# Performance work log

Measured on AMD Instinct MI355X. Metric: run time of the kernel, lower is better.

## Reference

```python
import jax, jax.numpy as jnp
import numpy as np


def _gcn_layer(ann, adj, Wa, ba, W2, b2):
    # ann: [B,N,F], adj: [B,E,N,N], Wa: [E,F,U], ba: [E,U], W2: [F,U], b2: [U]
    # per-edge-type linear, fused as one batched einsum -> [B,E,N,U]
    h = jnp.einsum('bnf,efu->benu', ann, Wa) + ba[None, :, None, :]
    # adjacency matmul per edge type: [B,E,N,N] @ [B,E,N,U]
    h = jnp.einsum('benm,bemu->benu', adj, h)
    # sum over edge types + residual linear + activation (tanh)
    out = h.sum(axis=1) + jnp.einsum('bnf,fu->bnu', ann, W2) + b2
    return jnp.tanh(out)


def setup_inputs() -> dict:
    key = jax.random.key(0)
    ks = jax.random.split(key, 10)
    B, N, F, E, U = 32, 1024, 32, 4, 32
    s = 1.0 / np.sqrt(F)
    s1 = 1.0 / np.sqrt(F + U)
    return {
        'n_tensor': jax.random.normal(ks[0], (B, N, F), dtype=jnp.float32),
        'adj_tensor': jax.random.uniform(ks[1], (B, E, N, N), dtype=jnp.float32),
        'W_adj0': jax.random.normal(ks[2], (E, F, U), dtype=jnp.float32) * s,
        'b_adj0': jax.random.normal(ks[3], (E, U), dtype=jnp.float32) * s,
        'W2_0': jax.random.normal(ks[4], (F, U), dtype=jnp.float32) * s,
        'b2_0': jax.random.normal(ks[5], (U,), dtype=jnp.float32) * s,
        'W_adj1': jax.random.normal(ks[6], (E, F + U, U), dtype=jnp.float32) * s1,
        'b_adj1': jax.random.normal(ks[7], (E, U), dtype=jnp.float32) * s1,
        'W2_1': jax.random.normal(ks[8], (F + U, U), dtype=jnp.float32) * s1,
        'b2_1': jax.random.normal(ks[9], (U,), dtype=jnp.float32) * s1,
    }


def reference(n_tensor, adj_tensor, W_adj0, b_adj0, W2_0, b2_0,
              W_adj1, b_adj1, W2_1, b2_1):
    # layer 0: h_tensor is None -> annotations = n_tensor
    h = _gcn_layer(n_tensor, adj_tensor, W_adj0, b_adj0, W2_0, b2_0)
    # layer 1: annotations = cat(n_tensor, hidden)
    ann1 = jnp.concatenate([n_tensor, h], axis=-1)
    h = _gcn_layer(ann1, adj_tensor, W_adj1, b_adj1, W2_1, b2_1)
    return h
```

## Files before the change

### kernel.cpp

```cpp
#include <hip/hip_runtime.h>
#include <math.h>

#define Nn 1024
#define Ee 4
#define Uu 32

template <int F, int FA>
__global__ __launch_bounds__(256) void pre_kernel(
    const float* __restrict__ annA, const float* __restrict__ annB,
    const float* __restrict__ Wa, const float* __restrict__ ba,
    const float* __restrict__ W2, const float* __restrict__ b2,
    float* __restrict__ hpre_t, float* __restrict__ res)
{
    const int e = blockIdx.y;
    __shared__ float wlds[F * Uu];
    __shared__ float blds[Uu];
    const int tid = threadIdx.x;
    const float* wsrc = (e < 4) ? (Wa + (size_t)e * F * Uu) : W2;
    const float* bsrc = (e < 4) ? (ba + (size_t)e * Uu) : b2;
    for (int i = tid; i < F * Uu; i += 256) wlds[i] = wsrc[i];
    if (tid < Uu) blds[tid] = bsrc[tid];
    __syncthreads();

    const int g = blockIdx.x * 256 + tid;
    const int b = g >> 10;
    const int n = g & 1023;

    float4 a4[F / 4];
    {
        const float4* rA = (const float4*)(annA + (size_t)g * FA);
#pragma unroll
        for (int i = 0; i < FA / 4; ++i) a4[i] = rA[i];
        if constexpr (F > FA) {
            const float4* rB = (const float4*)(annB + (size_t)g * (F - FA));
#pragma unroll
            for (int i = 0; i < (F - FA) / 4; ++i) a4[FA / 4 + i] = rB[i];
        }
    }

    float4 acc[8];
    const float4* bb = (const float4*)blds;
#pragma unroll
    for (int uq = 0; uq < 8; ++uq) acc[uq] = bb[uq];
    const float4* w4 = (const float4*)wlds;
#pragma unroll
    for (int f4 = 0; f4 < F / 4; ++f4) {
        const float4 av = a4[f4];
#pragma unroll
        for (int c = 0; c < 4; ++c) {
            const float s = (c == 0) ? av.x : (c == 1) ? av.y : (c == 2) ? av.z : av.w;
#pragma unroll
            for (int uq = 0; uq < 8; ++uq) {
                const float4 w = w4[(f4 * 4 + c) * 8 + uq];
                acc[uq].x = fmaf(s, w.x, acc[uq].x);
                acc[uq].y = fmaf(s, w.y, acc[uq].y);
                acc[uq].z = fmaf(s, w.z, acc[uq].z);
                acc[uq].w = fmaf(s, w.w, acc[uq].w);
            }
        }
    }
    if (e < 4) {
        float* dst = hpre_t + ((size_t)(b * 4 + e) * Uu) * Nn + n;
#pragma unroll
        for (int uq = 0; uq < 8; ++uq) {
            dst[(uq * 4 + 0) * Nn] = acc[uq].x;
            dst[(uq * 4 + 1) * Nn] = acc[uq].y;
            dst[(uq * 4 + 2) * Nn] = acc[uq].z;
            dst[(uq * 4 + 3) * Nn] = acc[uq].w;
        }
    } else {
        float4* dst = (float4*)(res + (size_t)g * Uu);
#pragma unroll
        for (int uq = 0; uq < 8; ++uq) dst[uq] = acc[uq];
    }
}

__global__ __launch_bounds__(256, 2) void gcn_main_kernel(
    const float* __restrict__ adj,
    const float* __restrict__ hpre_t,
    const float* __restrict__ res,
    float* __restrict__ out)
{
    __shared__ float part[4][8][Uu];

    const int bid = blockIdx.x;
    const int swz = (bid & 7) * 512 + (bid >> 3);
    const int b = swz >> 7;
    const int n0 = (swz & 127) * 8;
    const int tid = threadIdx.x;
    const int w = tid >> 6;
    const int lane = tid & 63;
    const int gu = lane >> 4;
    const int ms = lane & 15;

    const float* adjb = adj + (size_t)b * Ee * Nn * Nn;
    const float* hpb  = hpre_t + (size_t)b * Ee * Uu * Nn;
    const int mbase = w * 256 + ms * 4;

    float acc[8][8];
#pragma unroll
    for (int r = 0; r < 8; ++r)
#pragma unroll
        for (int j = 0; j < 8; ++j) acc[r][j] = 0.f;

#pragma unroll 2
    for (int it = 0; it < 16; ++it) {
        const int e = it >> 2, sub = it & 3;
        const float* ap = adjb + ((size_t)e * Nn + n0) * Nn + mbase + sub * 64;
        const float* hp = hpb + ((size_t)e * Uu + gu * 8) * Nn + mbase + sub * 64;
        float4 av[8], hv[8];
#pragma unroll
        for (int r = 0; r < 8; ++r) av[r] = *(const float4*)(ap + (size_t)r * Nn);
#pragma unroll
        for (int j = 0; j < 8; ++j) hv[j] = *(const float4*)(hp + (size_t)j * Nn);
#pragma unroll
        for (int j = 0; j < 8; ++j)
#pragma unroll
            for (int r = 0; r < 8; ++r) {
                float t0 = fmaf(av[r].x, hv[j].x, acc[r][j]);
                t0 = fmaf(av[r].y, hv[j].y, t0);
                t0 = fmaf(av[r].z, hv[j].z, t0);
                acc[r][j] = fmaf(av[r].w, hv[j].w, t0);
            }
    }

#pragma unroll
    for (int r = 0; r < 8; ++r)
#pragma unroll
        for (int j = 0; j < 8; ++j) {
            float v = acc[r][j];
            v += __shfl_xor(v, 1);
            v += __shfl_xor(v, 2);
            v += __shfl_xor(v, 4);
            v += __shfl_xor(v, 8);
            acc[r][j] = v;
        }

#pragma unroll
    for (int r = 0; r < 8; ++r) {
        if (ms == r) {
#pragma unroll
            for (int j = 0; j < 8; ++j) part[w][r][gu * 8 + j] = acc[r][j];
        }
    }
    __syncthreads();

    {
        const int r = tid >> 5, u = tid & 31;
        const float v = part[0][r][u] + part[1][r][u] + part[2][r][u] + part[3][r][u];
        const size_t oi = ((size_t)b * Nn + n0 + r) * Uu + u;
        out[oi] = tanhf(v + res[oi]);
    }
}

extern "C" void kernel_launch(void* const* d_in, const int* in_sizes, int n_in,
                              void* d_out, int out_size, void* d_ws, size_t ws_size,
                              hipStream_t stream)
{
    const float* n_tensor = (const float*)d_in[0];
    const float* adj      = (const float*)d_in[1];
    const float* W_adj0   = (const float*)d_in[2];
    const float* b_adj0   = (const float*)d_in[3];
    const float* W2_0     = (const float*)d_in[4];
    const float* b2_0     = (const float*)d_in[5];
    const float* W_adj1   = (const float*)d_in[6];
    const float* b_adj1   = (const float*)d_in[7];
    const float* W2_1     = (const float*)d_in[8];
    const float* b2_1     = (const float*)d_in[9];
    float* outp = (float*)d_out;

    float* ws   = (float*)d_ws;
    float* hpre = ws;
    float* resb = ws + (size_t)4 * 1024 * 1024;
    float* h0   = ws + (size_t)5 * 1024 * 1024;

    dim3 pre_grid(128, 5);

    pre_kernel<32, 32><<<pre_grid, 256, 0, stream>>>(n_tensor, nullptr, W_adj0, b_adj0,
                                                     W2_0, b2_0, hpre, resb);
    gcn_main_kernel<<<4096, 256, 0, stream>>>(adj, hpre, resb, h0);

    pre_kernel<64, 32><<<pre_grid, 256, 0, stream>>>(n_tensor, h0, W_adj1, b_adj1,
                                                     W2_1, b2_1, hpre, resb);
    gcn_main_kernel<<<4096, 256, 0, stream>>>(adj, hpre, resb, outp);
}
```

Baseline: 518.8 us.

## Stage hidden features in LDS and enlarge row tile per block

The adjacency-matmul kernel now processes 32 rows per 512-thread block. Each stage copies a 32x512 slice of the transformed hidden features into LDS with global_load_lds, and every wave reads it from there instead of re-fetching it from global memory. Each wave owns 4 full rows across all m, which removes the cross-wave LDS reduction and allows a vectorized tanh/residual epilogue. This cuts redundant h traffic but adds per-stage barriers and 64KB of LDS per block, which may limit occupancy. Adjacency streaming is unchanged.

```diff
diff --git a/kernel.cpp b/kernel.cpp
--- a/kernel.cpp
+++ b/kernel.cpp
@@ -4,6 +4,8 @@
 #define Nn 1024
 #define Ee 4
 #define Uu 32
+#define STAGE_M 512
+#define BLOCK_ROWS 32
 
 template <int F, int FA>
 __global__ __launch_bounds__(256) void pre_kernel(
@@ -75,57 +77,76 @@
     }
 }
 
-__global__ __launch_bounds__(256, 2) void gcn_main_kernel(
+__global__ __launch_bounds__(512, 4) void gcn_main_kernel(
     const float* __restrict__ adj,
     const float* __restrict__ hpre_t,
     const float* __restrict__ res,
     float* __restrict__ out)
 {
-    __shared__ float part[4][8][Uu];
+    __shared__ float hlds[Uu * STAGE_M];
 
     const int bid = blockIdx.x;
-    const int swz = (bid & 7) * 512 + (bid >> 3);
-    const int b = swz >> 7;
-    const int n0 = (swz & 127) * 8;
+    const int swz = (bid & 7) * 128 + (bid >> 3);
+    const int b = swz >> 5;
+    const int n0 = (swz & 31) * BLOCK_ROWS;
     const int tid = threadIdx.x;
     const int w = tid >> 6;
     const int lane = tid & 63;
     const int gu = lane >> 4;
     const int ms = lane & 15;
+    const int wrow = n0 + w * 4;
 
     const float* adjb = adj + (size_t)b * Ee * Nn * Nn;
     const float* hpb  = hpre_t + (size_t)b * Ee * Uu * Nn;
-    const int mbase = w * 256 + ms * 4;
-
-    float acc[8][8];
-#pragma unroll
-    for (int r = 0; r < 8; ++r)
+
+    float acc[4][8];
+#pragma unroll
+    for (int r = 0; r < 4; ++r)
 #pragma unroll
         for (int j = 0; j < 8; ++j) acc[r][j] = 0.f;
 
-#pragma unroll 2
-    for (int it = 0; it < 16; ++it) {
-        const int e = it >> 2, sub = it & 3;
-        const float* ap = adjb + ((size_t)e * Nn + n0) * Nn + mbase + sub * 64;
-        const float* hp = hpb + ((size_t)e * Uu + gu * 8) * Nn + mbase + sub * 64;
-        float4 av[8], hv[8];
-#pragma unroll
-        for (int r = 0; r < 8; ++r) av[r] = *(const float4*)(ap + (size_t)r * Nn);
-#pragma unroll
-        for (int j = 0; j < 8; ++j) hv[j] = *(const float4*)(hp + (size_t)j * Nn);
-#pragma unroll
-        for (int j = 0; j < 8; ++j)
-#pragma unroll
-            for (int r = 0; r < 8; ++r) {
-                float t0 = fmaf(av[r].x, hv[j].x, acc[r][j]);
-                t0 = fmaf(av[r].y, hv[j].y, t0);
-                t0 = fmaf(av[r].z, hv[j].z, t0);
-                acc[r][j] = fmaf(av[r].w, hv[j].w, t0);
+    for (int s = 0; s < 8; ++s) {
+        const int e = s >> 1;
+        const int m0 = (s & 1) * STAGE_M;
+
+        {
+            const float* hsrc = hpb + ((size_t)e * Uu + w * 4) * Nn + m0 + lane * 4;
+#pragma unroll
+            for (int uu = 0; uu < 4; ++uu) {
+#pragma unroll
+                for (int seg = 0; seg < 2; ++seg) {
+                    __builtin_amdgcn_global_load_lds(
+                        (const __attribute__((address_space(1))) void*)(hsrc + (size_t)uu * Nn + seg * 256),
+                        (__attribute__((address_space(3))) void*)(&hlds[(w * 4 + uu) * STAGE_M + seg * 256]),
+                        16, 0, 0);
+                }
             }
-    }
-
-#pragma unroll
-    for (int r = 0; r < 8; ++r)
+        }
+        __syncthreads();
+
+#pragma unroll
+        for (int c = 0; c < 8; ++c) {
+            const float* ap = adjb + ((size_t)e * Nn + wrow) * Nn + m0 + c * 64 + ms * 4;
+            float4 av[4];
+#pragma unroll
+            for (int r = 0; r < 4; ++r) av[r] = *(const float4*)(ap + (size_t)r * Nn);
+#pragma unroll
+            for (int j = 0; j < 8; ++j) {
+                const float4 hv = *(const float4*)(&hlds[(gu * 8 + j) * STAGE_M + c * 64 + ms * 4]);
+#pragma unroll
+                for (int r = 0; r < 4; ++r) {
+                    float t0 = fmaf(av[r].x, hv.x, acc[r][j]);
+                    t0 = fmaf(av[r].y, hv.y, t0);
+                    t0 = fmaf(av[r].z, hv.z, t0);
+                    acc[r][j] = fmaf(av[r].w, hv.w, t0);
+                }
+            }
+        }
+        __syncthreads();
+    }
+
+#pragma unroll
+    for (int r = 0; r < 4; ++r)
 #pragma unroll
         for (int j = 0; j < 8; ++j) {
             float v = acc[r][j];
@@ -137,19 +158,25 @@
         }
 
 #pragma unroll
-    for (int r = 0; r < 8; ++r) {
+    for (int r = 0; r < 4; ++r) {
         if (ms == r) {
-#pragma unroll
-            for (int j = 0; j < 8; ++j) part[w][r][gu * 8 + j] = acc[r][j];
-        }
-    }
-    __syncthreads();
-
-    {
-        const int r = tid >> 5, u = tid & 31;
-        const float v = part[0][r][u] + part[1][r][u] + part[2][r][u] + part[3][r][u];
-        const size_t oi = ((size_t)b * Nn + n0 + r) * Uu + u;
-        out[oi] = tanhf(v + res[oi]);
+            const int n = wrow + r;
+            const float* rp = res + ((size_t)b * Nn + n) * Uu + gu * 8;
+            float* op = out + ((size_t)b * Nn + n) * Uu + gu * 8;
+            const float4 r0 = *(const float4*)(rp);
+            const float4 r1 = *(const float4*)(rp + 4);
+            float4 o0, o1;
+            o0.x = tanhf(acc[r][0] + r0.x);
+            o0.y = tanhf(acc[r][1] + r0.y);
+            o0.z = tanhf(acc[r][2] + r0.z);
+            o0.w = tanhf(acc[r][3] + r0.w);
+            o1.x = tanhf(acc[r][4] + r1.x);
+            o1.y = tanhf(acc[r][5] + r1.y);
+            o1.z = tanhf(acc[r][6] + r1.z);
+            o1.w = tanhf(acc[r][7] + r1.w);
+            *(float4*)(op) = o0;
+            *(float4*)(op + 4) = o1;
+        }
     }
 }
 
@@ -178,9 +205,9 @@
 
     pre_kernel<32, 32><<<pre_grid, 256, 0, stream>>>(n_tensor, nullptr, W_adj0, b_adj0,
                                                      W2_0, b2_0, hpre, resb);
-    gcn_main_kernel<<<4096, 256, 0, stream>>>(adj, hpre, resb, h0);
+    gcn_main_kernel<<<1024, 512, 0, stream>>>(adj, hpre, resb, h0);
 
     pre_kernel<64, 32><<<pre_grid, 256, 0, stream>>>(n_tensor, h0, W_adj1, b_adj1,
                                                      W2_1, b2_1, hpre, resb);
-    gcn_main_kernel<<<4096, 256, 0, stream>>>(adj, hpre, resb, outp);
+    gcn_main_kernel<<<1024, 512, 0, stream>>>(adj, hpre, resb, outp);
 }
```

Result: faster. 445.2 us (-14.2%).

## Stage hidden features in LDS and widen GCN blocks to 32 adjacency rows

Applied to the files above, without the earlier changes.

The adjacency-matmul kernel now processes 32 output rows per block instead of 8, so it launches 1024 blocks instead of 4096. Each 256-column chunk of the transposed hidden features is staged in shared memory and shared by all four waves, with the next chunk prefetched into registers while the current one is consumed. This cuts the repeated L2/global reads of the hidden-feature matrix that every 8-row block used to make, leaving the kernel closer to being limited by streaming the adjacency tensor. In exchange each thread holds 64 accumulators, the kernel uses 32 KB of shared memory and two barriers per step, and the occupancy hint was dropped, which may lower occupancy and latency hiding.

```diff
diff --git a/kernel.cpp b/kernel.cpp
--- a/kernel.cpp
+++ b/kernel.cpp
@@ -4,6 +4,7 @@
 #define Nn 1024
 #define Ee 4
 #define Uu 32
+#define BLOCK_ROWS 32
 
 template <int F, int FA>
 __global__ __launch_bounds__(256) void pre_kernel(
@@ -75,81 +76,127 @@
     }
 }
 
-__global__ __launch_bounds__(256, 2) void gcn_main_kernel(
+__global__ __launch_bounds__(256) void gcn_main_kernel(
     const float* __restrict__ adj,
     const float* __restrict__ hpre_t,
     const float* __restrict__ res,
     float* __restrict__ out)
 {
-    __shared__ float part[4][8][Uu];
+    __shared__ float buf[Uu * 256];
 
     const int bid = blockIdx.x;
-    const int swz = (bid & 7) * 512 + (bid >> 3);
-    const int b = swz >> 7;
-    const int n0 = (swz & 127) * 8;
+    const int swz = (bid & 7) * 128 + (bid >> 3);
+    const int b = swz >> 5;
+    const int n0 = (swz & 31) * BLOCK_ROWS;
     const int tid = threadIdx.x;
     const int w = tid >> 6;
     const int lane = tid & 63;
-    const int gu = lane >> 4;
     const int ms = lane & 15;
+    const int rg = lane >> 4;
+    const int wrow = n0 + w * 8;
 
     const float* adjb = adj + (size_t)b * Ee * Nn * Nn;
     const float* hpb  = hpre_t + (size_t)b * Ee * Uu * Nn;
-    const int mbase = w * 256 + ms * 4;
-
-    float acc[8][8];
-#pragma unroll
-    for (int r = 0; r < 8; ++r)
-#pragma unroll
-        for (int j = 0; j < 8; ++j) acc[r][j] = 0.f;
-
-#pragma unroll 2
-    for (int it = 0; it < 16; ++it) {
-        const int e = it >> 2, sub = it & 3;
-        const float* ap = adjb + ((size_t)e * Nn + n0) * Nn + mbase + sub * 64;
-        const float* hp = hpb + ((size_t)e * Uu + gu * 8) * Nn + mbase + sub * 64;
-        float4 av[8], hv[8];
-#pragma unroll
-        for (int r = 0; r < 8; ++r) av[r] = *(const float4*)(ap + (size_t)r * Nn);
-#pragma unroll
-        for (int j = 0; j < 8; ++j) hv[j] = *(const float4*)(hp + (size_t)j * Nn);
-#pragma unroll
-        for (int j = 0; j < 8; ++j)
-#pragma unroll
-            for (int r = 0; r < 8; ++r) {
-                float t0 = fmaf(av[r].x, hv[j].x, acc[r][j]);
-                t0 = fmaf(av[r].y, hv[j].y, t0);
-                t0 = fmaf(av[r].z, hv[j].z, t0);
-                acc[r][j] = fmaf(av[r].w, hv[j].w, t0);
+
+    const int uh = tid >> 3, qb = tid & 7;
+    float4* buf4 = (float4*)buf;
+
+    float accA[32], accB[32];
+#pragma unroll
+    for (int u = 0; u < 32; ++u) { accA[u] = 0.f; accB[u] = 0.f; }
+
+    float4 hr[8];
+
+    {
+        const float* hs = hpb + (size_t)uh * Nn + qb * 4;
+#pragma unroll
+        for (int k = 0; k < 8; ++k) hr[k] = *(const float4*)(hs + k * 32);
+    }
+
+    for (int s = 0; s < 16; ++s) {
+        const int e = s >> 2, mq = s & 3;
+
+        asm volatile("s_waitcnt lgkmcnt(0)" ::: "memory");
+        __builtin_amdgcn_s_barrier();
+
+#pragma unroll
+        for (int k = 0; k < 8; ++k) buf4[uh * 64 + qb + 8 * k] = hr[k];
+
+        {
+            const int s2 = (s < 15) ? s + 1 : 15;
+            const int e2 = s2 >> 2, mq2 = s2 & 3;
+            const float* hs = hpb + ((size_t)e2 * Uu + uh) * Nn + mq2 * 256 + qb * 4;
+#pragma unroll
+            for (int k = 0; k < 8; ++k) hr[k] = *(const float4*)(hs + k * 32);
+        }
+
+        const float* ap0 = adjb + ((size_t)e * Nn + wrow + rg) * Nn + mq * 256 + ms * 4;
+        float4 a00 = *(const float4*)(ap0);
+        float4 a01 = *(const float4*)(ap0 + 4 * Nn);
+        __builtin_amdgcn_sched_barrier(0);
+
+        asm volatile("s_waitcnt lgkmcnt(0)" ::: "memory");
+        __builtin_amdgcn_s_barrier();
+        __builtin_amdgcn_sched_barrier(0);
+
+#pragma unroll
+        for (int c = 0; c < 4; ++c) {
+            float4 av0, av1;
+            if (c == 0) { av0 = a00; av1 = a01; }
+            else {
+                const float* ap = ap0 + c * 64;
+                av0 = *(const float4*)(ap);
+                av1 = *(const float4*)(ap + 4 * Nn);
             }
-    }
-
-#pragma unroll
-    for (int r = 0; r < 8; ++r)
-#pragma unroll
-        for (int j = 0; j < 8; ++j) {
-            float v = acc[r][j];
-            v += __shfl_xor(v, 1);
-            v += __shfl_xor(v, 2);
-            v += __shfl_xor(v, 4);
-            v += __shfl_xor(v, 8);
-            acc[r][j] = v;
-        }
-
-#pragma unroll
-    for (int r = 0; r < 8; ++r) {
-        if (ms == r) {
-#pragma unroll
-            for (int j = 0; j < 8; ++j) part[w][r][gu * 8 + j] = acc[r][j];
-        }
-    }
-    __syncthreads();
-
-    {
-        const int r = tid >> 5, u = tid & 31;
-        const float v = part[0][r][u] + part[1][r][u] + part[2][r][u] + part[3][r][u];
-        const size_t oi = ((size_t)b * Nn + n0 + r) * Uu + u;
-        out[oi] = tanhf(v + res[oi]);
+#pragma unroll
+            for (int u = 0; u < 32; ++u) {
+                const float4 hv = buf4[u * 64 + c * 16 + ms];
+                accA[u] = fmaf(av0.x, hv.x, fmaf(av0.y, hv.y,
+                           fmaf(av0.z, hv.z, fmaf(av0.w, hv.w, accA[u]))));
+                accB[u] = fmaf(av1.x, hv.x, fmaf(av1.y, hv.y,
+                           fmaf(av1.z, hv.z, fmaf(av1.w, hv.w, accB[u]))));
+            }
+        }
+    }
+
+#pragma unroll
+    for (int u = 0; u < 32; ++u) {
+        float v = accA[u];
+        v += __shfl_xor(v, 1);
+        v += __shfl_xor(v, 2);
+        v += __shfl_xor(v, 4);
+        v += __shfl_xor(v, 8);
+        accA[u] = v;
+        float v2 = accB[u];
+        v2 += __shfl_xor(v2, 1);
+        v2 += __shfl_xor(v2, 2);
+        v2 += __shfl_xor(v2, 4);
+        v2 += __shfl_xor(v2, 8);
+        accB[u] = v2;
+    }
+
+    if (ms == 0) {
+        const int r0 = wrow + rg, r1 = wrow + rg + 4;
+        const float4* rp0 = (const float4*)(res + ((size_t)b * Nn + r0) * Uu);
+        const float4* rp1 = (const float4*)(res + ((size_t)b * Nn + r1) * Uu);
+        float4* op0 = (float4*)(out + ((size_t)b * Nn + r0) * Uu);
+        float4* op1 = (float4*)(out + ((size_t)b * Nn + r1) * Uu);
+#pragma unroll
+        for (int q = 0; q < 8; ++q) {
+            const float4 rv0 = rp0[q];
+            const float4 rv1 = rp1[q];
+            float4 o0, o1;
+            o0.x = tanhf(accA[q * 4 + 0] + rv0.x);
+            o0.y = tanhf(accA[q * 4 + 1] + rv0.y);
+            o0.z = tanhf(accA[q * 4 + 2] + rv0.z);
+            o0.w = tanhf(accA[q * 4 + 3] + rv0.w);
+            o1.x = tanhf(accB[q * 4 + 0] + rv1.x);
+            o1.y = tanhf(accB[q * 4 + 1] + rv1.y);
+            o1.z = tanhf(accB[q * 4 + 2] + rv1.z);
+            o1.w = tanhf(accB[q * 4 + 3] + rv1.w);
+            op0[q] = o0;
+            op1[q] = o1;
+        }
     }
 }
 
@@ -178,9 +225,9 @@
 
     pre_kernel<32, 32><<<pre_grid, 256, 0, stream>>>(n_tensor, nullptr, W_adj0, b_adj0,
                                                      W2_0, b2_0, hpre, resb);
-    gcn_main_kernel<<<4096, 256, 0, stream>>>(adj, hpre, resb, h0);
+    gcn_main_kernel<<<1024, 256, 0, stream>>>(adj, hpre, resb, h0);
 
     pre_kernel<64, 32><<<pre_grid, 256, 0, stream>>>(n_tensor, h0, W_adj1, b_adj1,
                                                      W2_1, b2_1, hpre, resb);
-    gcn_main_kernel<<<4096, 256, 0, stream>>>(adj, hpre, resb, outp);
+    gcn_main_kernel<<<1024, 256, 0, stream>>>(adj, hpre, resb, outp);
 }
```

After: 996.3 us. +92.0%, slower.
